# Kernel optimization log

Measured on AMD Instinct MI355X. Metric: run time of the kernel, lower is better.

The kernel has to match this reference:

```python
import jax, jax.numpy as jnp
import numpy as np
import math

C = 512
B, T = 8, 2048
STRIDE = 2
LN_EPS = 1e-5
EPS = 1e-8


def _ln(x, g, b):
    mu = jnp.mean(x, axis=-1, keepdims=True)
    var = jnp.mean(jnp.square(x - mu), axis=-1, keepdims=True)
    return (x - mu) * jax.lax.rsqrt(var + LN_EPS) * g + b


def _lin(x, w, b):
    # torch Linear: y = x @ W^T + b, W: [out, in]
    return jnp.einsum('btc,oc->bto', x, w) + b


def setup_inputs() -> dict:
    key = jax.random.key(0)
    ks = iter(jax.random.split(key, 40))
    s = 0.02
    d = {'x': jax.random.normal(next(ks), (B, T, C), jnp.float32)}
    # downsample conv: [C_out, C_in, K]
    d['dw'] = jax.random.normal(next(ks), (C, C, 3), jnp.float32) * s
    d['db'] = jnp.zeros((C,), jnp.float32)
    for br in ('cr', 'd', 'c'):
        for p in ('q', 'k', 'v'):
            d[f'w{p}_{br}'] = jax.random.normal(next(ks), (C, C), jnp.float32) * s
            d[f'b{p}_{br}'] = jnp.zeros((C,), jnp.float32)
        d[f'ln_{br}_g'] = jnp.ones((C,), jnp.float32)
        d[f'ln_{br}_b'] = jnp.zeros((C,), jnp.float32)
    d['temp'] = jnp.asarray(0.1, jnp.float32)
    d['gw'] = jax.random.normal(next(ks), (3, 3 * C), jnp.float32) * s  # conv1d k=1 squeezed
    d['gb'] = jnp.zeros((3,), jnp.float32)
    return d


def _forward(x, dw, db, wq_cr, bq_cr, wk_cr, bk_cr, wv_cr, bv_cr, ln_cr_g, ln_cr_b,
             wq_d, bq_d, wk_d, bk_d, wv_d, bv_d, ln_d_g, ln_d_b,
             wq_c, bq_c, wk_c, bk_c, wv_c, bv_c, ln_c_g, ln_c_b,
             temp, gw, gb):
    scale = 1.0 / math.sqrt(C)
    # downsample: Conv1d(k=3, stride, pad=1) on [B,C,T]
    xc = jnp.transpose(x, (0, 2, 1))
    xd = jax.lax.conv_general_dilated(
        xc, dw, window_strides=(STRIDE,), padding=[(1, 1)],
        dimension_numbers=('NCH', 'OIH', 'NCH')) + db[None, :, None]
    x_down = jnp.transpose(xd, (0, 2, 1))  # [B, T//2, C]

    # cross-resolution branch
    q = _lin(x, wq_cr, bq_cr)
    k = _lin(x_down, wk_cr, bk_cr)
    v = _lin(x_down, wv_cr, bv_cr)
    a = jax.nn.softmax(jnp.einsum('btc,bsc->bts', q, k) * scale, axis=-1)
    out_cross = _ln(jnp.einsum('bts,bsc->btc', a, v), ln_cr_g, ln_cr_b)

    # dot-product branch
    q = _lin(x, wq_d, bq_d)
    k = _lin(x, wk_d, bk_d)
    v = _lin(x, wv_d, bv_d)
    a = jax.nn.softmax(jnp.einsum('btc,bsc->bts', q, k) * scale, axis=-1)
    out_dot = _ln(jnp.einsum('bts,bsc->btc', a, v), ln_d_g, ln_d_b)

    # cosine branch with learnable temperature
    q = _lin(x, wq_c, bq_c)
    k = _lin(x, wk_c, bk_c)
    qn = q / (jnp.linalg.norm(q, axis=2, keepdims=True) + EPS)
    kn = k / (jnp.linalg.norm(k, axis=2, keepdims=True) + EPS)
    t = jnp.maximum(temp, 0.01)
    a = jax.nn.softmax(jnp.einsum('btc,bsc->bts', qn, kn) / t, axis=-1)
    v = _lin(x, wv_c, bv_c)
    out_cos = _ln(jnp.einsum('bts,bsc->btc', a, v), ln_c_g, ln_c_b)

    # learned gating fusion (conv1d k=1 == per-position linear over 3C)
    fused = jnp.concatenate([out_cross, out_dot, out_cos], axis=-1)  # [B,T,3C]
    gate = jax.nn.softmax(jnp.einsum('btc,gc->btg', fused, gw) + gb, axis=-1)  # [B,T,3]
    z = (gate[..., 0:1] * out_cross + gate[..., 1:2] * out_dot + gate[..., 2:3] * out_cos)
    return z


def reference(x, dw, db, wq_cr, bq_cr, wk_cr, bk_cr, wv_cr, bv_cr, ln_cr_g, ln_cr_b,
              wq_d, bq_d, wk_d, bk_d, wv_d, bv_d, ln_d_g, ln_d_b,
              wq_c, bq_c, wk_c, bk_c, wv_c, bv_c, ln_c_g, ln_c_b,
              temp, gw, gb):
    return _forward(x, dw, db, wq_cr, bq_cr, wk_cr, bk_cr, wv_cr, bv_cr, ln_cr_g, ln_cr_b,
                    wq_d, bq_d, wk_d, bk_d, wv_d, bv_d, ln_d_g, ln_d_b,
                    wq_c, bq_c, wk_c, bk_c, wv_c, bv_c, ln_c_g, ln_c_b,
                    temp, gw, gb)
```

## Files before the change

kernel.cpp:

```cpp
#include <hip/hip_runtime.h>


typedef __attribute__((ext_vector_type(8))) __bf16 bf16x8;
typedef __attribute__((ext_vector_type(4))) float f32x4;

#define CDIM 512
#define TFULL 2048

#define GLL16(gp, lp)                                                        \
  __builtin_amdgcn_global_load_lds(                                          \
      (const __attribute__((address_space(1))) unsigned int*)(gp),           \
      (__attribute__((address_space(3))) unsigned int*)(lp), 16, 0, 0)

__device__ __forceinline__ unsigned short f2bf(float f) {
  unsigned u = __float_as_uint(f);
  u = (u + 0x7fffu + ((u >> 16) & 1u)) >> 16;
  return (unsigned short)u;
}
__device__ __forceinline__ float bf2f(unsigned short h) {
  return __uint_as_float(((unsigned)h) << 16);
}

__global__ __launch_bounds__(256)
void k_tobf16(const float* __restrict__ src, unsigned short* __restrict__ dst, long n4) {
  long i = (long)blockIdx.x * 256 + threadIdx.x;
  if (i >= n4) return;
  float4 f = reinterpret_cast<const float4*>(src)[i];
  unsigned short o4[4] = {f2bf(f.x), f2bf(f.y), f2bf(f.z), f2bf(f.w)};
  reinterpret_cast<uint2*>(dst)[i] = *reinterpret_cast<const uint2*>(o4);
}

struct WPtrs { const float* p[9]; };
__global__ __launch_bounds__(256)
void k_tobf16w(WPtrs w, unsigned short* __restrict__ dst) {
  int idx = blockIdx.x * 256 + threadIdx.x;
  if (idx >= 9 * 65536) return;
  int m = idx >> 16, off = idx & 65535;
  float4 f = reinterpret_cast<const float4*>(w.p[m])[off];
  unsigned short o4[4] = {f2bf(f.x), f2bf(f.y), f2bf(f.z), f2bf(f.w)};
  reinterpret_cast<uint2*>(dst + (long)m * 262144)[off] = *reinterpret_cast<const uint2*>(o4);
}

__global__ __launch_bounds__(256)
void k_dwreorder(const float* __restrict__ dw, unsigned short* __restrict__ dwb) {
  int idx = blockIdx.x * 256 + threadIdx.x;
  if (idx >= 512 * 1536) return;
  int o = idx / 1536, rem = idx - o * 1536;
  int k = rem >> 9, i = rem & 511;
  dwb[idx] = f2bf(dw[(o * 512 + i) * 3 + k]);
}

__global__ __launch_bounds__(256)
void k_fix(const unsigned short* __restrict__ XB, const unsigned short* __restrict__ DWB,
           const float* __restrict__ db, unsigned short* __restrict__ XD) {
  const int lane = threadIdx.x & 63, wave = threadIdx.x >> 6;
  const int idx = blockIdx.x * 4 + wave;
  const int b = idx >> 9, o = idx & 511;
  const unsigned short* xr = XB + (long)b * TFULL * CDIM + lane * 16;
  const unsigned short* wr = DWB + (long)o * 1536 + 512 + lane * 16;
  float acc = 0.f;
  uint4 xv0 = *reinterpret_cast<const uint4*>(xr);
  uint4 xv1 = *reinterpret_cast<const uint4*>(xr + 8);
  uint4 wv0 = *reinterpret_cast<const uint4*>(wr);
  uint4 wv1 = *reinterpret_cast<const uint4*>(wr + 8);
  const unsigned short* xp0 = (const unsigned short*)&xv0;
  const unsigned short* xp1 = (const unsigned short*)&xv1;
  const unsigned short* wp0 = (const unsigned short*)&wv0;
  const unsigned short* wp1 = (const unsigned short*)&wv1;
#pragma unroll
  for (int j = 0; j < 8; ++j) acc += bf2f(xp0[j]) * bf2f(wp0[j]);
#pragma unroll
  for (int j = 0; j < 8; ++j) acc += bf2f(xp1[j]) * bf2f(wp1[j]);
#pragma unroll
  for (int off = 32; off > 0; off >>= 1) acc += __shfl_xor(acc, off);
  if (lane == 0) XD[(long)b * 1024 * 512 + o] = f2bf(acc + db[o]);
}

__global__ __launch_bounds__(256)
void k_gemm(const unsigned short* __restrict__ A,
            const unsigned short* __restrict__ B,
            void* __restrict__ Cp,
            int K, int lda, int ldb, int ldc,
            long sA, long sB, long sC,
            const float* __restrict__ bias,
            float alpha, const float* __restrict__ tempPtr,
            int mode, int ldct) {
  const int gx = gridDim.x;
  const int nwg = gx * gridDim.y;
  int wg = blockIdx.x + gx * blockIdx.y;
  wg = (wg & 7) * (nwg >> 3) + (wg >> 3);
  const int tm0 = (wg % gx) * 128, tn0 = (wg / gx) * 128;
  const int bz = blockIdx.z;
  const unsigned short* Ag = A + (long)bz * sA;
  const unsigned short* Bg = B + (long)bz * sB;

  __shared__ __align__(16) unsigned short smem[32768];

  const int tid = threadIdx.x;
  const int lane = tid & 63;
  const int wave = tid >> 6;
  const int wm = (wave >> 1) * 64, wn = (wave & 1) * 64;
  const int lrow = lane & 15, kq = lane >> 4;

  f32x4 acc[4][4];
#pragma unroll
  for (int i = 0; i < 4; ++i)
#pragma unroll
    for (int j = 0; j < 4; ++j) acc[i][j] = f32x4{0.f, 0.f, 0.f, 0.f};

  const int sr = tid >> 3;
  const int sj = (tid & 7) ^ (sr & 7);
  const unsigned short* aSrc = Ag + (long)(tm0 + sr) * lda + sj * 8;
  const unsigned short* bSrc = Bg + (long)(tn0 + sr) * ldb + sj * 8;

  const int nt = K >> 6;

#define STAGE(kt_, buf_)                                                     \
  {                                                                          \
    unsigned short* aD = smem + (buf_) * 8192 + wave * 512;                  \
    unsigned short* bD = smem + 16384 + (buf_) * 8192 + wave * 512;          \
    _Pragma("unroll")                                                        \
    for (int rd = 0; rd < 4; ++rd) {                                         \
      GLL16(aSrc + (kt_) + (long)rd * 32 * lda, aD + rd * 2048);             \
      GLL16(bSrc + (kt_) + (long)rd * 32 * ldb, bD + rd * 2048);             \
    }                                                                        \
  }

  STAGE(0, 0);

  const int xr = (lrow & 7) << 3;
  for (int t = 0; t < nt; ++t) {
    if (t + 1 < nt) {
      STAGE((t + 1) << 6, (t + 1) & 1);
      asm volatile("s_waitcnt vmcnt(8)" ::: "memory");
    } else {
      asm volatile("s_waitcnt vmcnt(0)" ::: "memory");
    }
    __builtin_amdgcn_s_barrier();
    __builtin_amdgcn_sched_barrier(0);
    const unsigned short* As_ = smem + (t & 1) * 8192;
    const unsigned short* Bs_ = smem + 16384 + (t & 1) * 8192;
    bf16x8 af[4][2], bfv[4][2];
#pragma unroll
    for (int mi = 0; mi < 4; ++mi)
#pragma unroll
      for (int ks = 0; ks < 2; ++ks)
        af[mi][ks] = *reinterpret_cast<const bf16x8*>(
            &As_[(wm + mi * 16 + lrow) * 64 + ((ks * 32 + kq * 8) ^ xr)]);
#pragma unroll
    for (int ni = 0; ni < 4; ++ni)
#pragma unroll
      for (int ks = 0; ks < 2; ++ks)
        bfv[ni][ks] = *reinterpret_cast<const bf16x8*>(
            &Bs_[(wn + ni * 16 + lrow) * 64 + ((ks * 32 + kq * 8) ^ xr)]);
#pragma unroll
    for (int mi = 0; mi < 4; ++mi)
#pragma unroll
      for (int ni = 0; ni < 4; ++ni) {
        acc[mi][ni] = __builtin_amdgcn_mfma_f32_16x16x32_bf16(af[mi][0], bfv[ni][0], acc[mi][ni], 0, 0, 0);
        acc[mi][ni] = __builtin_amdgcn_mfma_f32_16x16x32_bf16(af[mi][1], bfv[ni][1], acc[mi][ni], 0, 0, 0);
      }
    __builtin_amdgcn_sched_barrier(0);
    if (t + 1 < nt) __builtin_amdgcn_s_barrier();
  }
#undef STAGE

  if (tempPtr) alpha = 1.0f / fmaxf(*tempPtr, 0.01f);

  if (mode == 1) {
    unsigned short* Cb = (unsigned short*)Cp + (long)bz * sC;
#pragma unroll
    for (int mi = 0; mi < 4; ++mi) {
      int rg = tm0 + wm + mi * 16 + kq * 4;
#pragma unroll
      for (int ni = 0; ni < 4; ++ni) {
        int cg = tn0 + wn + ni * 16 + lrow;
        float bb = bias ? bias[cg] : 0.f;
        f32x4 v = acc[mi][ni];
#pragma unroll
        for (int r = 0; r < 4; ++r)
          Cb[(long)(rg + r) * ldc + cg] = f2bf(v[r] * alpha + bb);
      }
    }
  } else {
    unsigned short* Cb = (unsigned short*)Cp + (long)bz * sC;
#pragma unroll
    for (int mi = 0; mi < 4; ++mi) {
      int rg = tm0 + wm + mi * 16 + kq * 4;
#pragma unroll
      for (int ni = 0; ni < 4; ++ni) {
        int cg = tn0 + wn + ni * 16 + lrow;
        float bb = bias ? bias[cg] : 0.f;
        f32x4 v = acc[mi][ni];
#pragma unroll
        for (int r = 0; r < 4; ++r)
          Cb[(long)cg * ldct + (rg + r)] = f2bf(v[r] * alpha + bb);
      }
    }
  }
}

__global__ __launch_bounds__(512)
void k_gemm256(const unsigned short* __restrict__ A,
               const unsigned short* __restrict__ B,
               unsigned short* __restrict__ C,
               int K, int lda, int ldb, int ldc,
               long sA, long sB, long sC,
               float alpha, const float* __restrict__ tempPtr) {
  const int gx = gridDim.x;
  const int nwg = gx * gridDim.y;
  int wg = blockIdx.x + gx * blockIdx.y;
  wg = (wg & 7) * (nwg >> 3) + (wg >> 3);
  const int tm0 = (wg % gx) * 256, tn0 = (wg / gx) * 256;
  const unsigned short* Ag = A + (long)blockIdx.z * sA;
  const unsigned short* Bg = B + (long)blockIdx.z * sB;

  __shared__ __align__(16) unsigned short smem[32768];

  const int tid = threadIdx.x;
  const int lane = tid & 63;
  const int wave = tid >> 6;
  const int wm = (wave >> 2) * 128, wn = (wave & 3) * 64;
  const int lrow = lane & 15, kq = lane >> 4;

  f32x4 acc[8][4];
#pragma unroll
  for (int i = 0; i < 8; ++i)
#pragma unroll
    for (int j = 0; j < 4; ++j) acc[i][j] = f32x4{0.f, 0.f, 0.f, 0.f};

  const int srow = lane >> 2;
  const int sslot = (lane & 3) ^ ((lane >> 3) & 3);
  const unsigned short* aS0 = Ag + (long)(tm0 + wave * 16 + srow) * lda + sslot * 8;
  const unsigned short* aS1 = aS0 + 128L * lda;
  const unsigned short* bS0 = Bg + (long)(tn0 + wave * 16 + srow) * ldb + sslot * 8;
  const unsigned short* bS1 = bS0 + 128L * ldb;

  const int nt = K >> 5;

#define STAGE256(kt_, buf_)                                                  \
  {                                                                          \
    unsigned short* aD = smem + (buf_) * 8192 + wave * 512;                  \
    unsigned short* bD = smem + 16384 + (buf_) * 8192 + wave * 512;          \
    GLL16(aS0 + (kt_), aD);                                                  \
    GLL16(aS1 + (kt_), aD + 4096);                                           \
    GLL16(bS0 + (kt_), bD);                                                  \
    GLL16(bS1 + (kt_), bD + 4096);                                           \
  }

  STAGE256(0, 0);

  const int xr = ((lrow >> 1) & 3) << 3;
  for (int t = 0; t < nt; ++t) {
    if (t + 1 < nt) {
      STAGE256((t + 1) << 5, (t + 1) & 1);
      asm volatile("s_waitcnt vmcnt(4)" ::: "memory");
    } else {
      asm volatile("s_waitcnt vmcnt(0)" ::: "memory");
    }
    __builtin_amdgcn_s_barrier();
    __builtin_amdgcn_sched_barrier(0);
    const unsigned short* As_ = smem + (t & 1) * 8192;
    const unsigned short* Bs_ = smem + 16384 + (t & 1) * 8192;
    bf16x8 bfv[4];
#pragma unroll
    for (int ni = 0; ni < 4; ++ni)
      bfv[ni] = *reinterpret_cast<const bf16x8*>(
          &Bs_[(wn + ni * 16 + lrow) * 32 + ((kq * 8) ^ xr)]);
#pragma unroll
    for (int mi = 0; mi < 8; ++mi) {
      bf16x8 af = *reinterpret_cast<const bf16x8*>(
          &As_[(wm + mi * 16 + lrow) * 32 + ((kq * 8) ^ xr)]);
#pragma unroll
      for (int ni = 0; ni < 4; ++ni)
        acc[mi][ni] = __builtin_amdgcn_mfma_f32_16x16x32_bf16(af, bfv[ni], acc[mi][ni], 0, 0, 0);
    }
    __builtin_amdgcn_sched_barrier(0);
    if (t + 1 < nt) __builtin_amdgcn_s_barrier();
  }
#undef STAGE256

  if (tempPtr) alpha = 1.0f / fmaxf(*tempPtr, 0.01f);

  C += (long)blockIdx.z * sC;
#pragma unroll
  for (int mi = 0; mi < 8; ++mi) {
    int rg = tm0 + wm + mi * 16 + kq * 4;
#pragma unroll
    for (int ni = 0; ni < 4; ++ni) {
      int cg = tn0 + wn + ni * 16 + lrow;
      f32x4 v = acc[mi][ni];
#pragma unroll
      for (int r = 0; r < 4; ++r)
        C[(long)(rg + r) * ldc + cg] = f2bf(v[r] * alpha);
    }
  }
}

__global__ __launch_bounds__(256)
void k_softmax(unsigned short* __restrict__ S, int cols) {
  const long base = (long)blockIdx.x * cols;
  const int tid = threadIdx.x, lane = tid & 63, wave = tid >> 6;
  const int nv = cols >> 3;
  float f[8];
  float mx = -3.0e38f;
  if (tid < nv) {
    uint4 v = *reinterpret_cast<const uint4*>(S + base + tid * 8);
    const unsigned short* pv = (const unsigned short*)&v;
#pragma unroll
    for (int j = 0; j < 8; ++j) { f[j] = bf2f(pv[j]); mx = fmaxf(mx, f[j]); }
  }
  __shared__ float rmax[4], rsum[4];
#pragma unroll
  for (int o = 32; o > 0; o >>= 1) mx = fmaxf(mx, __shfl_down(mx, o));
  if (lane == 0) rmax[wave] = mx;
  __syncthreads();
  mx = fmaxf(fmaxf(rmax[0], rmax[1]), fmaxf(rmax[2], rmax[3]));
  float sum = 0.f;
  if (tid < nv) {
#pragma unroll
    for (int j = 0; j < 8; ++j) { f[j] = __expf(f[j] - mx); sum += f[j]; }
  }
#pragma unroll
  for (int o = 32; o > 0; o >>= 1) sum += __shfl_down(sum, o);
  if (lane == 0) rsum[wave] = sum;
  __syncthreads();
  const float inv = 1.0f / (rsum[0] + rsum[1] + rsum[2] + rsum[3]);
  if (tid < nv) {
    unsigned short o8[8];
#pragma unroll
    for (int j = 0; j < 8; ++j) o8[j] = f2bf(f[j] * inv);
    *reinterpret_cast<uint4*>(S + base + tid * 8) = *reinterpret_cast<const uint4*>(o8);
  }
}

__global__ __launch_bounds__(256)
void k_l2norm(unsigned short* __restrict__ Q, int ld) {
  const int lane = threadIdx.x & 63, wave = threadIdx.x >> 6;
  const long row = (long)blockIdx.x * 4 + wave;
  unsigned short* p = Q + row * ld + lane * 8;
  uint4 v = *reinterpret_cast<const uint4*>(p);
  const unsigned short* pv = (const unsigned short*)&v;
  float f[8]; float q = 0.f;
#pragma unroll
  for (int j = 0; j < 8; ++j) { f[j] = bf2f(pv[j]); q += f[j] * f[j]; }
#pragma unroll
  for (int o = 32; o > 0; o >>= 1) q += __shfl_xor(q, o);
  float sc = 1.0f / (sqrtf(q) + 1e-8f);
  unsigned short o8[8];
#pragma unroll
  for (int j = 0; j < 8; ++j) o8[j] = f2bf(f[j] * sc);
  *reinterpret_cast<uint4*>(p) = *reinterpret_cast<const uint4*>(o8);
}

__global__ __launch_bounds__(256)
void k_ln_bf(unsigned short* __restrict__ X, const float* __restrict__ g,
             const float* __restrict__ b) {
  const int lane = threadIdx.x & 63, wave = threadIdx.x >> 6;
  const long row = (long)blockIdx.x * 4 + wave;
  unsigned short* p = X + row * CDIM + lane * 8;
  uint4 v = *reinterpret_cast<const uint4*>(p);
  const unsigned short* pv = (const unsigned short*)&v;
  float f[8];
  float s = 0.f, q = 0.f;
#pragma unroll
  for (int j = 0; j < 8; ++j) { f[j] = bf2f(pv[j]); s += f[j]; q += f[j] * f[j]; }
#pragma unroll
  for (int o = 32; o > 0; o >>= 1) { s += __shfl_xor(s, o); q += __shfl_xor(q, o); }
  float mu = s * (1.f / 512.f);
  float var = q * (1.f / 512.f) - mu * mu;
  float rs = rsqrtf(var + 1e-5f);
  float gg[8], bb[8];
  *reinterpret_cast<float4*>(&gg[0]) = *reinterpret_cast<const float4*>(g + lane * 8);
  *reinterpret_cast<float4*>(&gg[4]) = *reinterpret_cast<const float4*>(g + lane * 8 + 4);
  *reinterpret_cast<float4*>(&bb[0]) = *reinterpret_cast<const float4*>(b + lane * 8);
  *reinterpret_cast<float4*>(&bb[4]) = *reinterpret_cast<const float4*>(b + lane * 8 + 4);
  unsigned short o8[8];
#pragma unroll
  for (int j = 0; j < 8; ++j) o8[j] = f2bf((f[j] - mu) * rs * gg[j] + bb[j]);
  *reinterpret_cast<uint4*>(p) = *reinterpret_cast<const uint4*>(o8);
}

__global__ __launch_bounds__(256)
void k_gate(const unsigned short* __restrict__ o0, const unsigned short* __restrict__ o1,
            const unsigned short* __restrict__ o2, const float* __restrict__ gw,
            const float* __restrict__ gb, float* __restrict__ out) {
  __shared__ float gws[3 * 1536];
  for (int i = threadIdx.x; i < 3 * 1536; i += 256) gws[i] = gw[i];
  __syncthreads();
  const int lane = threadIdx.x & 63, wave = threadIdx.x >> 6;
  const long pos = (long)blockIdx.x * 4 + wave;
  const long off = pos * CDIM + lane * 8;
  float a[8], bq[8], cq[8];
  {
    uint4 va = *reinterpret_cast<const uint4*>(o0 + off);
    uint4 vb = *reinterpret_cast<const uint4*>(o1 + off);
    uint4 vc = *reinterpret_cast<const uint4*>(o2 + off);
    const unsigned short* pa = (const unsigned short*)&va;
    const unsigned short* pb = (const unsigned short*)&vb;
    const unsigned short* pc = (const unsigned short*)&vc;
#pragma unroll
    for (int j = 0; j < 8; ++j) { a[j] = bf2f(pa[j]); bq[j] = bf2f(pb[j]); cq[j] = bf2f(pc[j]); }
  }
  float l0 = 0.f, l1 = 0.f, l2 = 0.f;
  const int ch = lane * 8;
#pragma unroll
  for (int j = 0; j < 8; ++j) {
    l0 += a[j] * gws[ch + j] + bq[j] * gws[512 + ch + j] + cq[j] * gws[1024 + ch + j];
    l1 += a[j] * gws[1536 + ch + j] + bq[j] * gws[2048 + ch + j] + cq[j] * gws[2560 + ch + j];
    l2 += a[j] * gws[3072 + ch + j] + bq[j] * gws[3584 + ch + j] + cq[j] * gws[4096 + ch + j];
  }
#pragma unroll
  for (int o = 32; o > 0; o >>= 1) {
    l0 += __shfl_xor(l0, o); l1 += __shfl_xor(l1, o); l2 += __shfl_xor(l2, o);
  }
  l0 += gb[0]; l1 += gb[1]; l2 += gb[2];
  float m = fmaxf(l0, fmaxf(l1, l2));
  float e0 = __expf(l0 - m), e1 = __expf(l1 - m), e2 = __expf(l2 - m);
  float inv = 1.f / (e0 + e1 + e2);
  float g0 = e0 * inv, g1 = e1 * inv, g2 = e2 * inv;
  float r[8];
#pragma unroll
  for (int j = 0; j < 8; ++j) r[j] = g0 * a[j] + g1 * bq[j] + g2 * cq[j];
  *reinterpret_cast<float4*>(out + off) = *reinterpret_cast<const float4*>(&r[0]);
  *reinterpret_cast<float4*>(out + off + 4) = *reinterpret_cast<const float4*>(&r[4]);
}

extern "C" void kernel_launch(void* const* d_in, const int* in_sizes, int n_in,
                              void* d_out, int out_size, void* d_ws, size_t ws_size,
                              hipStream_t stream) {
  (void)in_sizes; (void)n_in; (void)out_size;
  const float* x = (const float*)d_in[0];
  const float* dw = (const float*)d_in[1];
  const float* db = (const float*)d_in[2];
  WPtrs wp;
  wp.p[0] = (const float*)d_in[3];
  wp.p[1] = (const float*)d_in[11];
  wp.p[2] = (const float*)d_in[13];
  wp.p[3] = (const float*)d_in[19];
  wp.p[4] = (const float*)d_in[21];
  wp.p[5] = (const float*)d_in[15];
  wp.p[6] = (const float*)d_in[23];
  wp.p[7] = (const float*)d_in[5];
  wp.p[8] = (const float*)d_in[7];
  const float* bq_cr = (const float*)d_in[4];
  const float* bk_cr = (const float*)d_in[6];
  const float* bv_cr = (const float*)d_in[8];
  const float* ln_cr_g = (const float*)d_in[9];
  const float* ln_cr_b = (const float*)d_in[10];
  const float* bq_d = (const float*)d_in[12];
  const float* bk_d = (const float*)d_in[14];
  const float* bv_d = (const float*)d_in[16];
  const float* ln_d_g = (const float*)d_in[17];
  const float* ln_d_b = (const float*)d_in[18];
  const float* bq_c = (const float*)d_in[20];
  const float* bk_c = (const float*)d_in[22];
  const float* bv_c = (const float*)d_in[24];
  const float* ln_c_g = (const float*)d_in[25];
  const float* ln_c_b = (const float*)d_in[26];
  const float* temp = (const float*)d_in[27];
  const float* gw = (const float*)d_in[28];
  const float* gb = (const float*)d_in[29];

  if (ws_size < 240000000ULL) return;

  char* p = (char*)d_ws;
  auto alloc = [&](size_t bytes) {
    void* r = (void*)p;
    p += (bytes + 255) & ~(size_t)255;
    return r;
  };
  alloc(1024);
  unsigned short* XB  = (unsigned short*)alloc(16384L * 512 * 2);
  unsigned short* XD  = (unsigned short*)alloc(8192L * 512 * 2);
  unsigned short* WB  = (unsigned short*)alloc(9L * 262144 * 2);
  unsigned short* DWB = (unsigned short*)alloc(512L * 1536 * 2);
  unsigned short* QB  = (unsigned short*)alloc(16384L * 512 * 2);
  unsigned short* KB  = (unsigned short*)alloc(8192L * 512 * 2);
  unsigned short* VT  = (unsigned short*)alloc(512L * 16384 * 2);
  unsigned short* OUT0 = (unsigned short*)alloc(16384L * 512 * 2);
  unsigned short* OUT1 = (unsigned short*)alloc(16384L * 512 * 2);
  unsigned short* OUT2 = (unsigned short*)alloc(16384L * 512 * 2);
  unsigned short* QK2 = (unsigned short*)alloc(16384L * 1024 * 2);
  float* BC = (float*)alloc(2048 * 4);
  unsigned short* SB = (unsigned short*)alloc(8L * 2048 * 2048 * 2);

  const float scale = 0.044194173824159216f;

  auto gemm = [&](const unsigned short* A, const unsigned short* Bm, void* Cm,
                  int M, int N, int K, int lda, int ldb, int ldc,
                  int batch, long sA, long sB, long sC,
                  const float* bias, float alpha, const float* tp, int mode, int ldct) {
    dim3 g(M / 128, N / 128, batch);
    k_gemm<<<g, 256, 0, stream>>>(A, Bm, Cm, K, lda, ldb, ldc, sA, sB, sC,
                                  bias, alpha, tp, mode, ldct);
  };
  auto gemm256 = [&](const unsigned short* A, const unsigned short* Bm,
                     unsigned short* Cm, int M, int N, int K,
                     int lda, int ldb, int ldc, int batch,
                     long sA, long sB, long sC, float alpha, const float* tp) {
    dim3 g(M / 256, N / 256, batch);
    k_gemm256<<<g, 512, 0, stream>>>(A, Bm, Cm, K, lda, ldb, ldc, sA, sB, sC, alpha, tp);
  };

  k_tobf16<<<8192, 256, 0, stream>>>(x, XB, 16384L * 512 / 4);
  k_tobf16w<<<2304, 256, 0, stream>>>(wp, WB);
  k_dwreorder<<<3072, 256, 0, stream>>>(dw, DWB);
  hipMemcpyAsync(BC,        bq_d, 512 * 4, hipMemcpyDeviceToDevice, stream);
  hipMemcpyAsync(BC + 512,  bk_d, 512 * 4, hipMemcpyDeviceToDevice, stream);
  hipMemcpyAsync(BC + 1024, bq_c, 512 * 4, hipMemcpyDeviceToDevice, stream);
  hipMemcpyAsync(BC + 1536, bk_c, 512 * 4, hipMemcpyDeviceToDevice, stream);

  gemm(XB - 512, DWB, XD, 1024, 512, 1536, 1024, 1536, 512,
       8, 1048576L, 0, 524288L, db, 1.f, nullptr, 1, 0);
  k_fix<<<1024, 256, 0, stream>>>(XB, DWB, db, XD);

  gemm(XB, WB + 0 * 262144L, QB, 16384, 512, 512, 512, 512, 512, 1, 0, 0, 0,
       bq_cr, 1.f, nullptr, 1, 0);
  gemm(XD, WB + 7 * 262144L, KB, 8192, 512, 512, 512, 512, 512, 1, 0, 0, 0,
       bk_cr, 1.f, nullptr, 1, 0);
  gemm(XD, WB + 8 * 262144L, VT, 1024, 512, 512, 512, 512, 0, 8,
       1024L * 512, 0, 512L * 1024, bv_cr, 1.f, nullptr, 2, 1024);
  gemm256(QB, KB, SB, 2048, 1024, 512, 512, 512, 1024, 8,
          2048L * 512, 1024L * 512, 2048L * 1024, scale, nullptr);
  k_softmax<<<16384, 256, 0, stream>>>(SB, 1024);
  gemm(SB, VT, OUT0, 2048, 512, 1024, 1024, 1024, 512, 8,
       2048L * 1024, 512L * 1024, 2048L * 512, nullptr, 1.f, nullptr, 1, 0);
  k_ln_bf<<<4096, 256, 0, stream>>>(OUT0, ln_cr_g, ln_cr_b);

  gemm(XB, WB + 1 * 262144L, QK2, 16384, 1024, 512, 512, 512, 1024, 1, 0, 0, 0,
       BC, 1.f, nullptr, 1, 0);
  gemm(XB, WB + 5 * 262144L, VT, 2048, 512, 512, 512, 512, 0, 8,
       2048L * 512, 0, 512L * 2048, bv_d, 1.f, nullptr, 2, 2048);
  gemm256(QK2, QK2 + 512, SB, 2048, 2048, 512, 1024, 1024, 2048, 8,
          2048L * 1024, 2048L * 1024, 2048L * 2048, scale, nullptr);
  k_softmax<<<16384, 256, 0, stream>>>(SB, 2048);
  gemm(SB, VT, OUT1, 2048, 512, 2048, 2048, 2048, 512, 8,
       2048L * 2048, 512L * 2048, 2048L * 512, nullptr, 1.f, nullptr, 1, 0);
  k_ln_bf<<<4096, 256, 0, stream>>>(OUT1, ln_d_g, ln_d_b);

  gemm(XB, WB + 3 * 262144L, QK2, 16384, 1024, 512, 512, 512, 1024, 1, 0, 0, 0,
       BC + 1024, 1.f, nullptr, 1, 0);
  k_l2norm<<<4096, 256, 0, stream>>>(QK2, 1024);
  k_l2norm<<<4096, 256, 0, stream>>>(QK2 + 512, 1024);
  gemm(XB, WB + 6 * 262144L, VT, 2048, 512, 512, 512, 512, 0, 8,
       2048L * 512, 0, 512L * 2048, bv_c, 1.f, nullptr, 2, 2048);
  gemm256(QK2, QK2 + 512, SB, 2048, 2048, 512, 1024, 1024, 2048, 8,
          2048L * 1024, 2048L * 1024, 2048L * 2048, 1.f, temp);
  k_softmax<<<16384, 256, 0, stream>>>(SB, 2048);
  gemm(SB, VT, OUT2, 2048, 512, 2048, 2048, 2048, 512, 8,
       2048L * 2048, 512L * 2048, 2048L * 512, nullptr, 1.f, nullptr, 1, 0);
  k_ln_bf<<<4096, 256, 0, stream>>>(OUT2, ln_c_g, ln_c_b);

  k_gate<<<4096, 256, 0, stream>>>(OUT0, OUT1, OUT2, gw, gb, (float*)d_out);
}
```

Measured before the change: 561.8 us.

## Compute V^T as W·X^T GEMM and stage gemm256 epilogue through LDS

The V projection is now computed directly as a transposed product (W_v times X^T) over the whole batch, writing row-major V^T with coalesced stores and a per-row bias. This replaces the earlier transposed scatter epilogue, whose strided 2-byte stores were poorly coalesced. The 256-tile score GEMM epilogue now writes through swizzled shared memory in two passes and emits 16-byte vector stores, again replacing scattered 2-byte global writes. The PV GEMMs are re-pointed to the new V^T layout with batch strides into one wide matrix. The cost is extra shared-memory barriers in the epilogue and a different leading dimension for the V^T reads.

```diff
diff --git a/kernel.cpp b/kernel.cpp
--- a/kernel.cpp
+++ b/kernel.cpp
@@ -84,7 +84,7 @@
             long sA, long sB, long sC,
             const float* __restrict__ bias,
             float alpha, const float* __restrict__ tempPtr,
-            int mode, int ldct) {
+            int mode) {
   const int gx = gridDim.x;
   const int nwg = gx * gridDim.y;
   int wg = blockIdx.x + gx * blockIdx.y;
@@ -167,8 +167,8 @@
 
   if (tempPtr) alpha = 1.0f / fmaxf(*tempPtr, 0.01f);
 
+  unsigned short* Cb = (unsigned short*)Cp + (long)bz * sC;
   if (mode == 1) {
-    unsigned short* Cb = (unsigned short*)Cp + (long)bz * sC;
 #pragma unroll
     for (int mi = 0; mi < 4; ++mi) {
       int rg = tm0 + wm + mi * 16 + kq * 4;
@@ -183,18 +183,19 @@
       }
     }
   } else {
-    unsigned short* Cb = (unsigned short*)Cp + (long)bz * sC;
 #pragma unroll
     for (int mi = 0; mi < 4; ++mi) {
       int rg = tm0 + wm + mi * 16 + kq * 4;
+      float rb[4];
+#pragma unroll
+      for (int r = 0; r < 4; ++r) rb[r] = bias[rg + r];
 #pragma unroll
       for (int ni = 0; ni < 4; ++ni) {
         int cg = tn0 + wn + ni * 16 + lrow;
-        float bb = bias ? bias[cg] : 0.f;
         f32x4 v = acc[mi][ni];
 #pragma unroll
         for (int r = 0; r < 4; ++r)
-          Cb[(long)cg * ldct + (rg + r)] = f2bf(v[r] * alpha + bb);
+          Cb[(long)(rg + r) * ldc + cg] = f2bf(v[r] * alpha + rb[r]);
       }
     }
   }
@@ -283,17 +284,36 @@
   if (tempPtr) alpha = 1.0f / fmaxf(*tempPtr, 0.01f);
 
   C += (long)blockIdx.z * sC;
-#pragma unroll
-  for (int mi = 0; mi < 8; ++mi) {
-    int rg = tm0 + wm + mi * 16 + kq * 4;
-#pragma unroll
-    for (int ni = 0; ni < 4; ++ni) {
-      int cg = tn0 + wn + ni * 16 + lrow;
-      f32x4 v = acc[mi][ni];
-#pragma unroll
-      for (int r = 0; r < 4; ++r)
-        C[(long)(rg + r) * ldc + cg] = f2bf(v[r] * alpha);
+  unsigned short* eb = smem;
+  const int erow0 = (wm >> 1) + kq * 4;
+  const int ecol0 = wn + lrow;
+  const int orow = tid >> 2, oq = tid & 3;
+  const int oxr = orow & 7;
+#pragma unroll
+  for (int pass = 0; pass < 2; ++pass) {
+    __syncthreads();
+#pragma unroll
+    for (int mi2 = 0; mi2 < 4; ++mi2) {
+#pragma unroll
+      for (int ni = 0; ni < 4; ++ni) {
+        f32x4 v = acc[pass * 4 + mi2][ni];
+        const int col = ecol0 + ni * 16;
+        const int cs = col >> 3, cl = col & 7;
+#pragma unroll
+        for (int r = 0; r < 4; ++r) {
+          const int row = erow0 + mi2 * 16 + r;
+          eb[row * 256 + ((cs ^ (row & 7)) << 3) + cl] = f2bf(v[r] * alpha);
+        }
+      }
     }
+    __syncthreads();
+    const long grow = tm0 + pass * 64 + orow + (orow & 64);
+    unsigned short* dst = C + grow * ldc + tn0 + oq * 64;
+    const unsigned short* src = eb + orow * 256;
+#pragma unroll
+    for (int j = 0; j < 8; ++j)
+      *reinterpret_cast<uint4*>(dst + j * 8) =
+          *reinterpret_cast<const uint4*>(src + (((oq * 8 + j) ^ oxr) << 3));
   }
 }
 
@@ -490,10 +510,10 @@
   auto gemm = [&](const unsigned short* A, const unsigned short* Bm, void* Cm,
                   int M, int N, int K, int lda, int ldb, int ldc,
                   int batch, long sA, long sB, long sC,
-                  const float* bias, float alpha, const float* tp, int mode, int ldct) {
+                  const float* bias, float alpha, const float* tp, int mode) {
     dim3 g(M / 128, N / 128, batch);
     k_gemm<<<g, 256, 0, stream>>>(A, Bm, Cm, K, lda, ldb, ldc, sA, sB, sC,
-                                  bias, alpha, tp, mode, ldct);
+                                  bias, alpha, tp, mode);
   };
   auto gemm256 = [&](const unsigned short* A, const unsigned short* Bm,
                      unsigned short* Cm, int M, int N, int K,
@@ -512,44 +532,44 @@
   hipMemcpyAsync(BC + 1536, bk_c, 512 * 4, hipMemcpyDeviceToDevice, stream);
 
   gemm(XB - 512, DWB, XD, 1024, 512, 1536, 1024, 1536, 512,
-       8, 1048576L, 0, 524288L, db, 1.f, nullptr, 1, 0);
+       8, 1048576L, 0, 524288L, db, 1.f, nullptr, 1);
   k_fix<<<1024, 256, 0, stream>>>(XB, DWB, db, XD);
 
   gemm(XB, WB + 0 * 262144L, QB, 16384, 512, 512, 512, 512, 512, 1, 0, 0, 0,
-       bq_cr, 1.f, nullptr, 1, 0);
+       bq_cr, 1.f, nullptr, 1);
   gemm(XD, WB + 7 * 262144L, KB, 8192, 512, 512, 512, 512, 512, 1, 0, 0, 0,
-       bk_cr, 1.f, nullptr, 1, 0);
-  gemm(XD, WB + 8 * 262144L, VT, 1024, 512, 512, 512, 512, 0, 8,
-       1024L * 512, 0, 512L * 1024, bv_cr, 1.f, nullptr, 2, 1024);
+       bk_cr, 1.f, nullptr, 1);
+  gemm(WB + 8 * 262144L, XD, VT, 512, 8192, 512, 512, 512, 8192, 1, 0, 0, 0,
+       bv_cr, 1.f, nullptr, 3);
   gemm256(QB, KB, SB, 2048, 1024, 512, 512, 512, 1024, 8,
           2048L * 512, 1024L * 512, 2048L * 1024, scale, nullptr);
   k_softmax<<<16384, 256, 0, stream>>>(SB, 1024);
-  gemm(SB, VT, OUT0, 2048, 512, 1024, 1024, 1024, 512, 8,
-       2048L * 1024, 512L * 1024, 2048L * 512, nullptr, 1.f, nullptr, 1, 0);
+  gemm(SB, VT, OUT0, 2048, 512, 1024, 1024, 8192, 512, 8,
+       2048L * 1024, 1024, 2048L * 512, nullptr, 1.f, nullptr, 1);
   k_ln_bf<<<4096, 256, 0, stream>>>(OUT0, ln_cr_g, ln_cr_b);
 
   gemm(XB, WB + 1 * 262144L, QK2, 16384, 1024, 512, 512, 512, 1024, 1, 0, 0, 0,
-       BC, 1.f, nullptr, 1, 0);
-  gemm(XB, WB + 5 * 262144L, VT, 2048, 512, 512, 512, 512, 0, 8,
-       2048L * 512, 0, 512L * 2048, bv_d, 1.f, nullptr, 2, 2048);
+       BC, 1.f, nullptr, 1);
+  gemm(WB + 5 * 262144L, XB, VT, 512, 16384, 512, 512, 512, 16384, 1, 0, 0, 0,
+       bv_d, 1.f, nullptr, 3);
   gemm256(QK2, QK2 + 512, SB, 2048, 2048, 512, 1024, 1024, 2048, 8,
           2048L * 1024, 2048L * 1024, 2048L * 2048, scale, nullptr);
   k_softmax<<<16384, 256, 0, stream>>>(SB, 2048);
-  gemm(SB, VT, OUT1, 2048, 512, 2048, 2048, 2048, 512, 8,
-       2048L * 2048, 512L * 2048, 2048L * 512, nullptr, 1.f, nullptr, 1, 0);
+  gemm(SB, VT, OUT1, 2048, 512, 2048, 2048, 16384, 512, 8,
+       2048L * 2048, 2048, 2048L * 512, nullptr, 1.f, nullptr, 1);
   k_ln_bf<<<4096, 256, 0, stream>>>(OUT1, ln_d_g, ln_d_b);
 
   gemm(XB, WB + 3 * 262144L, QK2, 16384, 1024, 512, 512, 512, 1024, 1, 0, 0, 0,
-       BC + 1024, 1.f, nullptr, 1, 0);
+       BC + 1024, 1.f, nullptr, 1);
   k_l2norm<<<4096, 256, 0, stream>>>(QK2, 1024);
   k_l2norm<<<4096, 256, 0, stream>>>(QK2 + 512, 1024);
-  gemm(XB, WB + 6 * 262144L, VT, 2048, 512, 512, 512, 512, 0, 8,
-       2048L * 512, 0, 512L * 2048, bv_c, 1.f, nullptr, 2, 2048);
+  gemm(WB + 6 * 262144L, XB, VT, 512, 16384, 512, 512, 512, 16384, 1, 0, 0, 0,
+       bv_c, 1.f, nullptr, 3);
   gemm256(QK2, QK2 + 512, SB, 2048, 2048, 512, 1024, 1024, 2048, 8,
           2048L * 1024, 2048L * 1024, 2048L * 2048, 1.f, temp);
   k_softmax<<<16384, 256, 0, stream>>>(SB, 2048);
-  gemm(SB, VT, OUT2, 2048, 512, 2048, 2048, 2048, 512, 8,
-       2048L * 2048, 512L * 2048, 2048L * 512, nullptr, 1.f, nullptr, 1, 0);
+  gemm(SB, VT, OUT2, 2048, 512, 2048, 2048, 16384, 512, 8,
+       2048L * 2048, 2048, 2048L * 512, nullptr, 1.f, nullptr, 1);
   k_ln_bf<<<4096, 256, 0, stream>>>(OUT2, ln_c_g, ln_c_b);
 
   k_gate<<<4096, 256, 0, stream>>>(OUT0, OUT1, OUT2, gw, gb, (float*)d_out);
```

Result: slower. 626.0 us (+11.4%).
